# Performance work log

Measured on AMD Instinct MI355X. Metric: run time of the kernel, lower is better.

Reference implementation:

```python
import jax, jax.numpy as jnp
import numpy as np

B, I, D = 4096, 512, 2048
MAX_DIM = 2560
LEAK_RATE = 0.2
SPIKE_THRESHOLD = 0.5


def setup_inputs() -> dict:
    key = jax.random.key(0)
    k1, k2, k3, k4, k5 = jax.random.split(key, 5)
    return {
        "inputs": jax.random.normal(k1, (B, I), dtype=jnp.float32),
        "state": jax.random.normal(k2, (B, MAX_DIM), dtype=jnp.float32),
        "W_in": jax.random.normal(k3, (D, I), dtype=jnp.float32) * 0.05,
        "W_res": jax.random.normal(k4, (D, D), dtype=jnp.float32) * 0.02,
        "W_gate": jax.random.normal(k5, (3 * D, I), dtype=jnp.float32) * 0.05,
    }


def reference(inputs, state, W_in, W_res, W_gate):
    # Slice previous state to the active reservoir dimension D.
    prev_state = state[:, :D]                                   # [B, D]
    input_part = inputs @ W_in.T                                 # [B, D]
    reservoir_part = prev_state @ W_res.T                        # [B, D]
    gate_part = jax.nn.sigmoid(inputs @ W_gate.T)                # [B, 3D]
    i_gate, f_gate, o_gate = jnp.split(gate_part, 3, axis=-1)
    new_state = (1.0 - LEAK_RATE) * (f_gate * prev_state) \
        + LEAK_RATE * jnp.tanh(i_gate * (input_part + reservoir_part))
    new_state = o_gate * new_state
    # Spike thresholding: subtract threshold where state exceeds it.
    new_state = jnp.where(new_state > SPIKE_THRESHOLD,
                          new_state - SPIKE_THRESHOLD, new_state)
    # Zero-pad active reservoir back to max_dynamic_reservoir_dim.
    padded = jnp.pad(new_state, ((0, 0), (0, MAX_DIM - D)))      # [B, MAX_DIM]
    return padded
```

## Files before the change

kernel.cpp:

```cpp
#include <hip/hip_runtime.h>
#include <math.h>


#define IDIM 512
#define DDIM 2048
#define MAXD 2560
#define BDIM 4096
#define BCAP 96
#define OCAP 262144
#define BAND 4e-3f

typedef __attribute__((ext_vector_type(4))) float f32x4;
typedef __attribute__((ext_vector_type(8))) _Float16 f16x8;

__device__ __forceinline__ void gld16(const unsigned short* g, unsigned short* l) {
    __builtin_amdgcn_global_load_lds((const __attribute__((address_space(1))) void*)g,
                                     (__attribute__((address_space(3))) void*)l,
                                     16, 0, 0);
}
__device__ __forceinline__ float sigf(float x) { return 1.0f / (1.0f + __expf(-x)); }

__global__ __launch_bounds__(256) void convert_kernel(
    const float* __restrict__ x, const float* __restrict__ state,
    const float* __restrict__ win, const float* __restrict__ wgate,
    const float* __restrict__ wres,
    unsigned short* __restrict__ X16, unsigned short* __restrict__ S16,
    unsigned short* __restrict__ Wc16, unsigned short* __restrict__ Wr16,
    float* __restrict__ out, unsigned* __restrict__ cntA)
{
    int idx = blockIdx.x * 256 + threadIdx.x;
    if (idx < 2052) cntA[idx] = 0u;
    float4 v;
    unsigned short* p;
    long off;
    if (idx < 524288) {
        v = ((const float4*)x)[idx];
        p = X16; off = (long)idx * 4;
    } else if (idx < 2621440) {
        int i = idx - 524288;
        int row = i >> 9, c4 = i & 511;
        v = *(const float4*)(state + (long)row * MAXD + c4 * 4);
        p = S16; off = (long)i * 4;
    } else if (idx < 3670016) {
        int i = idx - 2621440;
        v = (i < 262144) ? ((const float4*)win)[i] : ((const float4*)wgate)[i - 262144];
        p = Wc16; off = (long)i * 4;
    } else if (idx < 4718592) {
        int i = idx - 3670016;
        v = ((const float4*)wres)[i];
        p = Wr16; off = (long)i * 4;
    } else {
        int i = idx - 4718592;
        int row = i >> 7, c4 = i & 127;
        *(float4*)(out + (long)row * MAXD + DDIM + c4 * 4) = make_float4(0.f, 0.f, 0.f, 0.f);
        return;
    }
    _Float16 h0 = (_Float16)v.x, h1 = (_Float16)v.y;
    _Float16 h2 = (_Float16)v.z, h3 = (_Float16)v.w;
    ushort4 hv;
    hv.x = *(unsigned short*)&h0; hv.y = *(unsigned short*)&h1;
    hv.z = *(unsigned short*)&h2; hv.w = *(unsigned short*)&h3;
    *(ushort4*)(p + off) = hv;
}

__global__ __launch_bounds__(512, 4) void fused_step(
    const unsigned short* __restrict__ X16, const unsigned short* __restrict__ S16,
    const unsigned short* __restrict__ Wc16, const unsigned short* __restrict__ Wr16,
    const float* __restrict__ state, float* __restrict__ out,
    unsigned* __restrict__ cntA, unsigned* __restrict__ bl, unsigned* __restrict__ ol)
{
    __shared__ alignas(16) unsigned short lA[128 * 32];
    __shared__ alignas(16) unsigned short lB[128 * 32];
    const int t = threadIdx.x;
    const int wave = t >> 6, lane = t & 63;
    const int wm = wave >> 2, wn = wave & 3;
    const int quad = lane >> 4, l16 = lane & 15;

    const int bid = blockIdx.x;
    const int nb  = (bid & 7) * 64 + (bid >> 3);
    const int xcd = nb >> 6, lid = nb & 63;
    const int m0 = (((xcd >> 1) << 3) + (lid >> 3)) * 128;
    const int n0 = (((xcd & 1) << 3) + (lid & 7)) * 128;

    const int rowoff = lane >> 2;
    const int kg = ((lane & 3) ^ ((lane >> 3) & 3)) * 8;
    const int krh = (quad ^ ((l16 >> 1) & 3)) * 8;

    f32x4 acc[4][2];
    f32x4 u[4][2];

    #pragma unroll
    for (int mi = 0; mi < 4; mi++)
        #pragma unroll
        for (int ni = 0; ni < 2; ni++)
            acc[mi][ni] = (f32x4)0.0f;

    auto phase = [&](const unsigned short* Ag, long ldA,
                     const unsigned short* Bg, long ldB, int klen) {
        const unsigned short* a0 = Ag + (long)(wave * 16 + rowoff) * ldA + kg;
        const unsigned short* b0 = Bg + (long)(wave * 16 + rowoff) * ldB + kg;
        unsigned short* dA = lA + wave * 512;
        unsigned short* dB = lB + wave * 512;
        for (int k0 = 0; k0 < klen; k0 += 32) {
            __syncthreads();
            gld16(a0 + k0, dA);
            gld16(b0 + k0, dB);
            __syncthreads();
            f16x8 af[4], bf[2];
            #pragma unroll
            for (int mi = 0; mi < 4; mi++)
                af[mi] = *(const f16x8*)&lA[(wm * 64 + mi * 16 + l16) * 32 + krh];
            #pragma unroll
            for (int ni = 0; ni < 2; ni++)
                bf[ni] = *(const f16x8*)&lB[(wn * 32 + ni * 16 + l16) * 32 + krh];
            #pragma unroll
            for (int mi = 0; mi < 4; mi++)
                #pragma unroll
                for (int ni = 0; ni < 2; ni++)
                    acc[mi][ni] = __builtin_amdgcn_mfma_f32_16x16x32_f16(af[mi], bf[ni], acc[mi][ni], 0, 0, 0);
        }
    };

    phase(S16 + (long)m0 * DDIM, DDIM, Wr16 + (long)n0 * DDIM, DDIM, DDIM);
    phase(X16 + (long)m0 * IDIM, IDIM, Wc16 + (long)n0 * IDIM, IDIM, IDIM);
    #pragma unroll
    for (int mi = 0; mi < 4; mi++)
        #pragma unroll
        for (int ni = 0; ni < 2; ni++) { u[mi][ni] = acc[mi][ni]; acc[mi][ni] = (f32x4)0.0f; }

    phase(X16 + (long)m0 * IDIM, IDIM, Wc16 + (long)(DDIM + n0) * IDIM, IDIM, IDIM);
    #pragma unroll
    for (int mi = 0; mi < 4; mi++)
        #pragma unroll
        for (int ni = 0; ni < 2; ni++) {
            #pragma unroll
            for (int r = 0; r < 4; r++)
                u[mi][ni][r] = 0.2f * tanhf(sigf(acc[mi][ni][r]) * u[mi][ni][r]);
            acc[mi][ni] = (f32x4)0.0f;
        }

    phase(X16 + (long)m0 * IDIM, IDIM, Wc16 + (long)(2 * DDIM + n0) * IDIM, IDIM, IDIM);
    #pragma unroll
    for (int mi = 0; mi < 4; mi++)
        #pragma unroll
        for (int ni = 0; ni < 2; ni++) {
            #pragma unroll
            for (int r = 0; r < 4; r++) {
                int row = m0 + wm * 64 + mi * 16 + quad * 4 + r;
                int col = n0 + wn * 32 + ni * 16 + l16;
                float prev = state[(long)row * MAXD + col];
                u[mi][ni][r] += 0.8f * sigf(acc[mi][ni][r]) * prev;
            }
            acc[mi][ni] = (f32x4)0.0f;
        }

    #pragma unroll
    for (int mi = 0; mi < 4; mi++)
        (void)0;
    phase(X16 + (long)m0 * IDIM, IDIM, Wc16 + (long)(3 * DDIM + n0) * IDIM, IDIM, IDIM);
    #pragma unroll
    for (int mi = 0; mi < 4; mi++)
        #pragma unroll
        for (int ni = 0; ni < 2; ni++) {
            #pragma unroll
            for (int r = 0; r < 4; r++) {
                int row = m0 + wm * 64 + mi * 16 + quad * 4 + r;
                int col = n0 + wn * 32 + ni * 16 + l16;
                float go = sigf(acc[mi][ni][r]);
                float ns = go * u[mi][ni][r];
                float ov = (ns > 0.5f) ? ns - 0.5f : ns;
                out[(long)row * MAXD + col] = ov;
                if (fabsf(ns - 0.5f) < BAND) {
                    unsigned pos = atomicAdd(&cntA[col], 1u);
                    if (pos < BCAP) {
                        bl[col * BCAP + pos] = (unsigned)row;
                    } else {
                        unsigned op = atomicAdd(&cntA[2048], 1u);
                        if (op < OCAP) ol[op] = (unsigned)((row << 11) | col);
                    }
                }
            }
        }
}

__global__ __launch_bounds__(256) void fixup_kernel(
    const float* __restrict__ x, const float* __restrict__ state,
    const float* __restrict__ win, const float* __restrict__ wres,
    const float* __restrict__ wgate,
    const unsigned* __restrict__ cntA, const unsigned* __restrict__ bl,
    const unsigned* __restrict__ ol, float* __restrict__ out)
{
    __shared__ float sWin[512], sWi[512], sWf[512], sWo[512];
    __shared__ float sWr[2048];
    const int c = blockIdx.x;
    const int t = threadIdx.x;
    const int wave = t >> 6, lane = t & 63;

    unsigned m = cntA[c]; if (m > BCAP) m = BCAP;
    if (m > 0) {
        for (int k = t; k < 512; k += 256) {
            sWin[k] = win[(long)c * IDIM + k];
            sWi[k]  = wgate[(long)c * IDIM + k];
            sWf[k]  = wgate[(long)(DDIM + c) * IDIM + k];
            sWo[k]  = wgate[(long)(2 * DDIM + c) * IDIM + k];
        }
        for (int k = t; k < 2048; k += 256)
            sWr[k] = wres[(long)c * DDIM + k];
        __syncthreads();

        for (unsigned e = wave; e < m; e += 4) {
            int row = (int)bl[c * BCAP + e];
            double ip = 0.0, gi = 0.0, gf = 0.0, go = 0.0, rp = 0.0;
            const float* xr = x + (long)row * IDIM;
            #pragma unroll 2
            for (int k = lane * 4; k < IDIM; k += 256) {
                float4 xv = *(const float4*)(xr + k);
                ip += (double)xv.x * (double)sWin[k]   + (double)xv.y * (double)sWin[k+1]
                    + (double)xv.z * (double)sWin[k+2] + (double)xv.w * (double)sWin[k+3];
                gi += (double)xv.x * (double)sWi[k]    + (double)xv.y * (double)sWi[k+1]
                    + (double)xv.z * (double)sWi[k+2]  + (double)xv.w * (double)sWi[k+3];
                gf += (double)xv.x * (double)sWf[k]    + (double)xv.y * (double)sWf[k+1]
                    + (double)xv.z * (double)sWf[k+2]  + (double)xv.w * (double)sWf[k+3];
                go += (double)xv.x * (double)sWo[k]    + (double)xv.y * (double)sWo[k+1]
                    + (double)xv.z * (double)sWo[k+2]  + (double)xv.w * (double)sWo[k+3];
            }
            const float* sr = state + (long)row * MAXD;
            #pragma unroll 4
            for (int k = lane * 4; k < DDIM; k += 256) {
                float4 sv = *(const float4*)(sr + k);
                rp += (double)sv.x * (double)sWr[k]   + (double)sv.y * (double)sWr[k+1]
                    + (double)sv.z * (double)sWr[k+2] + (double)sv.w * (double)sWr[k+3];
            }
            #pragma unroll
            for (int o = 32; o > 0; o >>= 1) {
                ip += __shfl_down(ip, o);
                gi += __shfl_down(gi, o);
                gf += __shfl_down(gf, o);
                go += __shfl_down(go, o);
                rp += __shfl_down(rp, o);
            }
            if (lane == 0) {
                double si = 1.0 / (1.0 + exp(-gi));
                double sf = 1.0 / (1.0 + exp(-gf));
                double so = 1.0 / (1.0 + exp(-go));
                double prev = (double)state[(long)row * MAXD + c];
                double ns = so * (0.8 * sf * prev + 0.2 * tanh(si * (ip + rp)));
                if (ns > 0.5) ns -= 0.5;
                out[(long)row * MAXD + c] = (float)ns;
            }
        }
    }

    unsigned nof = cntA[2048]; if (nof > OCAP) nof = OCAP;
    const int gw = blockIdx.x * 4 + wave;
    for (unsigned e = gw; e < nof; e += 2048 * 4) {
        unsigned rc = ol[e];
        int row = (int)(rc >> 11), col = (int)(rc & 2047);
        double ip = 0.0, gi = 0.0, gf = 0.0, go = 0.0, rp = 0.0;
        const float* xr  = x + (long)row * IDIM;
        const float* wi  = win + (long)col * IDIM;
        const float* wgi = wgate + (long)col * IDIM;
        const float* wgf = wgate + (long)(DDIM + col) * IDIM;
        const float* wgo = wgate + (long)(2 * DDIM + col) * IDIM;
        for (int k = lane * 4; k < IDIM; k += 256) {
            float4 xv = *(const float4*)(xr + k);
            float4 a = *(const float4*)(wi + k);
            float4 b = *(const float4*)(wgi + k);
            float4 cc = *(const float4*)(wgf + k);
            float4 d = *(const float4*)(wgo + k);
            ip += (double)xv.x * a.x + (double)xv.y * a.y + (double)xv.z * a.z + (double)xv.w * a.w;
            gi += (double)xv.x * b.x + (double)xv.y * b.y + (double)xv.z * b.z + (double)xv.w * b.w;
            gf += (double)xv.x * cc.x + (double)xv.y * cc.y + (double)xv.z * cc.z + (double)xv.w * cc.w;
            go += (double)xv.x * d.x + (double)xv.y * d.y + (double)xv.z * d.z + (double)xv.w * d.w;
        }
        const float* sr = state + (long)row * MAXD;
        const float* wr_ = wres + (long)col * DDIM;
        for (int k = lane * 4; k < DDIM; k += 256) {
            float4 sv = *(const float4*)(sr + k);
            float4 wv = *(const float4*)(wr_ + k);
            rp += (double)sv.x * wv.x + (double)sv.y * wv.y + (double)sv.z * wv.z + (double)sv.w * wv.w;
        }
        #pragma unroll
        for (int o = 32; o > 0; o >>= 1) {
            ip += __shfl_down(ip, o);
            gi += __shfl_down(gi, o);
            gf += __shfl_down(gf, o);
            go += __shfl_down(go, o);
            rp += __shfl_down(rp, o);
        }
        if (lane == 0) {
            double si = 1.0 / (1.0 + exp(-gi));
            double sf = 1.0 / (1.0 + exp(-gf));
            double so = 1.0 / (1.0 + exp(-go));
            double prev = (double)state[(long)row * MAXD + col];
            double ns = so * (0.8 * sf * prev + 0.2 * tanh(si * (ip + rp)));
            if (ns > 0.5) ns -= 0.5;
            out[(long)row * MAXD + col] = (float)ns;
        }
    }
}

extern "C" void kernel_launch(void* const* d_in, const int* in_sizes, int n_in,
                              void* d_out, int out_size, void* d_ws, size_t ws_size,
                              hipStream_t stream) {
    const float* x     = (const float*)d_in[0];
    const float* state = (const float*)d_in[1];
    const float* win   = (const float*)d_in[2];
    const float* wres  = (const float*)d_in[3];
    const float* wgate = (const float*)d_in[4];
    float* out = (float*)d_out;

    char* ws = (char*)d_ws;
    unsigned short* X16  = (unsigned short*)(ws);
    unsigned short* S16  = (unsigned short*)(ws + (4ll  << 20));
    unsigned short* Wc16 = (unsigned short*)(ws + (20ll << 20));
    unsigned short* Wr16 = (unsigned short*)(ws + (28ll << 20));
    unsigned* cntA = (unsigned*)(ws + (36ll << 20));
    unsigned* bl   = (unsigned*)(ws + (36ll << 20) + (16ll << 10));
    unsigned* ol   = (unsigned*)(ws + (37ll << 20));

    convert_kernel<<<dim3(20480), dim3(256), 0, stream>>>(
        x, state, win, wgate, wres, X16, S16, Wc16, Wr16, out, cntA);

    fused_step<<<dim3(512), dim3(512), 0, stream>>>(
        X16, S16, Wc16, Wr16, state, out, cntA, bl, ol);

    fixup_kernel<<<dim3(2048), dim3(256), 0, stream>>>(
        x, state, win, wres, wgate, cntA, bl, ol, out);
}
```

Before: 336.4 us.

## Fuse near-threshold fp64 fixup into GEMM epilogue with LDS work list

Near-threshold elements are now collected in a per-block LDS list instead of global per-column lists. The same GEMM block then recomputes them in double precision right after its epilogue, reusing lA as the list buffer. A small overflow kernel handles entries beyond the LDS capacity. This removes the separate 2048-block fixup pass and the global per-column atomics, but fixups now read weight rows straight from global memory rather than per-column LDS copies, and they lengthen the tail of the GEMM blocks.

New measurement: 321.2 us. -4.5%, faster.

```diff
diff --git a/kernel.cpp b/kernel.cpp
--- a/kernel.cpp
+++ b/kernel.cpp
@@ -6,7 +6,7 @@
 #define DDIM 2048
 #define MAXD 2560
 #define BDIM 4096
-#define BCAP 96
+#define FCAP 2048
 #define OCAP 262144
 #define BAND 4e-3f
 
@@ -26,10 +26,10 @@
     const float* __restrict__ wres,
     unsigned short* __restrict__ X16, unsigned short* __restrict__ S16,
     unsigned short* __restrict__ Wc16, unsigned short* __restrict__ Wr16,
-    float* __restrict__ out, unsigned* __restrict__ cntA)
+    float* __restrict__ out, unsigned* __restrict__ cnt)
 {
     int idx = blockIdx.x * 256 + threadIdx.x;
-    if (idx < 2052) cntA[idx] = 0u;
+    if (idx == 0) *cnt = 0u;
     float4 v;
     unsigned short* p;
     long off;
@@ -66,15 +66,19 @@
 __global__ __launch_bounds__(512, 4) void fused_step(
     const unsigned short* __restrict__ X16, const unsigned short* __restrict__ S16,
     const unsigned short* __restrict__ Wc16, const unsigned short* __restrict__ Wr16,
-    const float* __restrict__ state, float* __restrict__ out,
-    unsigned* __restrict__ cntA, unsigned* __restrict__ bl, unsigned* __restrict__ ol)
+    const float* __restrict__ x, const float* __restrict__ state,
+    const float* __restrict__ win, const float* __restrict__ wres,
+    const float* __restrict__ wgate, float* __restrict__ out,
+    unsigned* __restrict__ gcnt, unsigned* __restrict__ ol)
 {
     __shared__ alignas(16) unsigned short lA[128 * 32];
     __shared__ alignas(16) unsigned short lB[128 * 32];
+    __shared__ unsigned scnt;
     const int t = threadIdx.x;
     const int wave = t >> 6, lane = t & 63;
     const int wm = wave >> 2, wn = wave & 3;
     const int quad = lane >> 4, l16 = lane & 15;
+    if (t == 0) scnt = 0u;
 
     const int bid = blockIdx.x;
     const int nb  = (bid & 7) * 64 + (bid >> 3);
@@ -154,10 +158,11 @@
             acc[mi][ni] = (f32x4)0.0f;
         }
 
-    #pragma unroll
-    for (int mi = 0; mi < 4; mi++)
-        (void)0;
     phase(X16 + (long)m0 * IDIM, IDIM, Wc16 + (long)(3 * DDIM + n0) * IDIM, IDIM, IDIM);
+
+    __syncthreads();
+    unsigned* flg = (unsigned*)lA;
+
     #pragma unroll
     for (int mi = 0; mi < 4; mi++)
         #pragma unroll
@@ -171,89 +176,80 @@
                 float ov = (ns > 0.5f) ? ns - 0.5f : ns;
                 out[(long)row * MAXD + col] = ov;
                 if (fabsf(ns - 0.5f) < BAND) {
-                    unsigned pos = atomicAdd(&cntA[col], 1u);
-                    if (pos < BCAP) {
-                        bl[col * BCAP + pos] = (unsigned)row;
+                    unsigned pos = atomicAdd(&scnt, 1u);
+                    if (pos < FCAP) {
+                        flg[pos] = (unsigned)((row << 11) | col);
                     } else {
-                        unsigned op = atomicAdd(&cntA[2048], 1u);
+                        unsigned op = atomicAdd(gcnt, 1u);
                         if (op < OCAP) ol[op] = (unsigned)((row << 11) | col);
                     }
                 }
             }
         }
-}
-
-__global__ __launch_bounds__(256) void fixup_kernel(
+
+    __syncthreads();
+    unsigned nf = scnt; if (nf > FCAP) nf = FCAP;
+
+    for (unsigned e = wave; e < nf; e += 8) {
+        unsigned rc = flg[e];
+        int row = (int)(rc >> 11), col = (int)(rc & 2047);
+        double ip = 0.0, gi = 0.0, gf = 0.0, go = 0.0, rp = 0.0;
+        const float* xr  = x + (long)row * IDIM;
+        const float* wi  = win + (long)col * IDIM;
+        const float* wgi = wgate + (long)col * IDIM;
+        const float* wgf = wgate + (long)(DDIM + col) * IDIM;
+        const float* wgo = wgate + (long)(2 * DDIM + col) * IDIM;
+        for (int k = lane * 4; k < IDIM; k += 256) {
+            float4 xv = *(const float4*)(xr + k);
+            float4 a = *(const float4*)(wi + k);
+            float4 b = *(const float4*)(wgi + k);
+            float4 c = *(const float4*)(wgf + k);
+            float4 d = *(const float4*)(wgo + k);
+            ip += (double)xv.x * a.x + (double)xv.y * a.y + (double)xv.z * a.z + (double)xv.w * a.w;
+            gi += (double)xv.x * b.x + (double)xv.y * b.y + (double)xv.z * b.z + (double)xv.w * b.w;
+            gf += (double)xv.x * c.x + (double)xv.y * c.y + (double)xv.z * c.z + (double)xv.w * c.w;
+            go += (double)xv.x * d.x + (double)xv.y * d.y + (double)xv.z * d.z + (double)xv.w * d.w;
+        }
+        const float* sr = state + (long)row * MAXD;
+        const float* wr_ = wres + (long)col * DDIM;
+        for (int k = lane * 4; k < DDIM; k += 256) {
+            float4 sv = *(const float4*)(sr + k);
+            float4 wv = *(const float4*)(wr_ + k);
+            rp += (double)sv.x * wv.x + (double)sv.y * wv.y + (double)sv.z * wv.z + (double)sv.w * wv.w;
+        }
+        #pragma unroll
+        for (int o = 32; o > 0; o >>= 1) {
+            ip += __shfl_down(ip, o);
+            gi += __shfl_down(gi, o);
+            gf += __shfl_down(gf, o);
+            go += __shfl_down(go, o);
+            rp += __shfl_down(rp, o);
+        }
+        if (lane == 0) {
+            double si = 1.0 / (1.0 + exp(-gi));
+            double sf = 1.0 / (1.0 + exp(-gf));
+            double so = 1.0 / (1.0 + exp(-go));
+            double prev = (double)state[(long)row * MAXD + col];
+            double ns = so * (0.8 * sf * prev + 0.2 * tanh(si * (ip + rp)));
+            if (ns > 0.5) ns -= 0.5;
+            out[(long)row * MAXD + col] = (float)ns;
+        }
+    }
+}
+
+__global__ __launch_bounds__(256) void overflow_kernel(
     const float* __restrict__ x, const float* __restrict__ state,
     const float* __restrict__ win, const float* __restrict__ wres,
     const float* __restrict__ wgate,
-    const unsigned* __restrict__ cntA, const unsigned* __restrict__ bl,
-    const unsigned* __restrict__ ol, float* __restrict__ out)
+    const unsigned* __restrict__ gcnt, const unsigned* __restrict__ ol,
+    float* __restrict__ out)
 {
-    __shared__ float sWin[512], sWi[512], sWf[512], sWo[512];
-    __shared__ float sWr[2048];
-    const int c = blockIdx.x;
-    const int t = threadIdx.x;
-    const int wave = t >> 6, lane = t & 63;
-
-    unsigned m = cntA[c]; if (m > BCAP) m = BCAP;
-    if (m > 0) {
-        for (int k = t; k < 512; k += 256) {
-            sWin[k] = win[(long)c * IDIM + k];
-            sWi[k]  = wgate[(long)c * IDIM + k];
-            sWf[k]  = wgate[(long)(DDIM + c) * IDIM + k];
-            sWo[k]  = wgate[(long)(2 * DDIM + c) * IDIM + k];
-        }
-        for (int k = t; k < 2048; k += 256)
-            sWr[k] = wres[(long)c * DDIM + k];
-        __syncthreads();
-
-        for (unsigned e = wave; e < m; e += 4) {
-            int row = (int)bl[c * BCAP + e];
-            double ip = 0.0, gi = 0.0, gf = 0.0, go = 0.0, rp = 0.0;
-            const float* xr = x + (long)row * IDIM;
-            #pragma unroll 2
-            for (int k = lane * 4; k < IDIM; k += 256) {
-                float4 xv = *(const float4*)(xr + k);
-                ip += (double)xv.x * (double)sWin[k]   + (double)xv.y * (double)sWin[k+1]
-                    + (double)xv.z * (double)sWin[k+2] + (double)xv.w * (double)sWin[k+3];
-                gi += (double)xv.x * (double)sWi[k]    + (double)xv.y * (double)sWi[k+1]
-                    + (double)xv.z * (double)sWi[k+2]  + (double)xv.w * (double)sWi[k+3];
-                gf += (double)xv.x * (double)sWf[k]    + (double)xv.y * (double)sWf[k+1]
-                    + (double)xv.z * (double)sWf[k+2]  + (double)xv.w * (double)sWf[k+3];
-                go += (double)xv.x * (double)sWo[k]    + (double)xv.y * (double)sWo[k+1]
-                    + (double)xv.z * (double)sWo[k+2]  + (double)xv.w * (double)sWo[k+3];
-            }
-            const float* sr = state + (long)row * MAXD;
-            #pragma unroll 4
-            for (int k = lane * 4; k < DDIM; k += 256) {
-                float4 sv = *(const float4*)(sr + k);
-                rp += (double)sv.x * (double)sWr[k]   + (double)sv.y * (double)sWr[k+1]
-                    + (double)sv.z * (double)sWr[k+2] + (double)sv.w * (double)sWr[k+3];
-            }
-            #pragma unroll
-            for (int o = 32; o > 0; o >>= 1) {
-                ip += __shfl_down(ip, o);
-                gi += __shfl_down(gi, o);
-                gf += __shfl_down(gf, o);
-                go += __shfl_down(go, o);
-                rp += __shfl_down(rp, o);
-            }
-            if (lane == 0) {
-                double si = 1.0 / (1.0 + exp(-gi));
-                double sf = 1.0 / (1.0 + exp(-gf));
-                double so = 1.0 / (1.0 + exp(-go));
-                double prev = (double)state[(long)row * MAXD + c];
-                double ns = so * (0.8 * sf * prev + 0.2 * tanh(si * (ip + rp)));
-                if (ns > 0.5) ns -= 0.5;
-                out[(long)row * MAXD + c] = (float)ns;
-            }
-        }
-    }
-
-    unsigned nof = cntA[2048]; if (nof > OCAP) nof = OCAP;
-    const int gw = blockIdx.x * 4 + wave;
-    for (unsigned e = gw; e < nof; e += 2048 * 4) {
+    const int gwave = (blockIdx.x * 256 + threadIdx.x) >> 6;
+    const int lane = threadIdx.x & 63;
+    const int nwaves = gridDim.x * 4;
+    unsigned n = *gcnt;
+    if (n > OCAP) n = OCAP;
+    for (unsigned e = gwave; e < n; e += nwaves) {
         unsigned rc = ol[e];
         int row = (int)(rc >> 11), col = (int)(rc & 2047);
         double ip = 0.0, gi = 0.0, gf = 0.0, go = 0.0, rp = 0.0;
@@ -266,11 +262,11 @@
             float4 xv = *(const float4*)(xr + k);
             float4 a = *(const float4*)(wi + k);
             float4 b = *(const float4*)(wgi + k);
-            float4 cc = *(const float4*)(wgf + k);
+            float4 c = *(const float4*)(wgf + k);
             float4 d = *(const float4*)(wgo + k);
             ip += (double)xv.x * a.x + (double)xv.y * a.y + (double)xv.z * a.z + (double)xv.w * a.w;
             gi += (double)xv.x * b.x + (double)xv.y * b.y + (double)xv.z * b.z + (double)xv.w * b.w;
-            gf += (double)xv.x * cc.x + (double)xv.y * cc.y + (double)xv.z * cc.z + (double)xv.w * cc.w;
+            gf += (double)xv.x * c.x + (double)xv.y * c.y + (double)xv.z * c.z + (double)xv.w * c.w;
             go += (double)xv.x * d.x + (double)xv.y * d.y + (double)xv.z * d.z + (double)xv.w * d.w;
         }
         const float* sr = state + (long)row * MAXD;
@@ -315,16 +311,15 @@
     unsigned short* S16  = (unsigned short*)(ws + (4ll  << 20));
     unsigned short* Wc16 = (unsigned short*)(ws + (20ll << 20));
     unsigned short* Wr16 = (unsigned short*)(ws + (28ll << 20));
-    unsigned* cntA = (unsigned*)(ws + (36ll << 20));
-    unsigned* bl   = (unsigned*)(ws + (36ll << 20) + (16ll << 10));
-    unsigned* ol   = (unsigned*)(ws + (37ll << 20));
+    unsigned* gcnt = (unsigned*)(ws + (36ll << 20));
+    unsigned* ol   = (unsigned*)(ws + (36ll << 20) + 16);
 
     convert_kernel<<<dim3(20480), dim3(256), 0, stream>>>(
-        x, state, win, wgate, wres, X16, S16, Wc16, Wr16, out, cntA);
+        x, state, win, wgate, wres, X16, S16, Wc16, Wr16, out, gcnt);
 
     fused_step<<<dim3(512), dim3(512), 0, stream>>>(
-        X16, S16, Wc16, Wr16, state, out, cntA, bl, ol);
-
-    fixup_kernel<<<dim3(2048), dim3(256), 0, stream>>>(
-        x, state, win, wres, wgate, cntA, bl, ol, out);
-}
+        X16, S16, Wc16, Wr16, x, state, win, wres, wgate, out, gcnt, ol);
+
+    overflow_kernel<<<dim3(128), dim3(256), 0, stream>>>(
+        x, state, win, wres, wgate, gcnt, ol, out);
+}
```
